# Performance work log

Hardware: AMD Instinct MI355X
Metric: run time of the kernel (lower is better)

The kernel has to match this reference:

```python
import jax, jax.numpy as jnp
import numpy as np

# Model hyperparameters (match init_kwargs)
C_IN = 256      # in_channels
H = 8           # n_heads
CH = 16         # hid_channels
FQ = 8          # freq_bins
WIN = 100       # window_size
VH = C_IN // H                  # 32, v_hid_channels
CT = H * (2 * CH + VH)          # 512, qkv conv out channels
HD = CH * FQ                    # 128, head_dim
VHD = VH * FQ                   # 256, v_head_dim
EPS = 1e-5


def _prelu(x, a):
    return jnp.where(x >= 0, x, a * x)


def _chan_ln(x, g, b):
    # LayerNormalization4D: normalize over channel dim (axis=1) of [B, Ch, D1, D2]
    mu = jnp.mean(x, axis=1, keepdims=True)
    var = jnp.var(x, axis=1, keepdims=True)
    return (x - mu) * jax.lax.rsqrt(var + EPS) * g[None, :, None, None] + b[None, :, None, None]


def setup_inputs() -> dict:
    key = jax.random.key(0)
    ks = jax.random.split(key, 8)
    B, T = 4, 1000
    x = jax.random.normal(ks[0], (B, C_IN, FQ, T), dtype=jnp.float32)
    w_qkv = jax.random.normal(ks[1], (CT, C_IN), dtype=jnp.float32) * 0.02
    b_qkv = jnp.zeros((CT,), dtype=jnp.float32)
    a_qkv = jnp.float32(0.25)
    g_qkv = jnp.ones((CT,), dtype=jnp.float32)
    be_qkv = jnp.zeros((CT,), dtype=jnp.float32)
    w_proj = jax.random.normal(ks[2], (C_IN, C_IN), dtype=jnp.float32) * 0.02
    b_proj = jnp.zeros((C_IN,), dtype=jnp.float32)
    a_proj = jnp.float32(0.25)
    g_proj = jnp.ones((C_IN,), dtype=jnp.float32)
    be_proj = jnp.zeros((C_IN,), dtype=jnp.float32)
    return {"x": x, "w_qkv": w_qkv, "b_qkv": b_qkv, "a_qkv": a_qkv, "g_qkv": g_qkv,
            "be_qkv": be_qkv, "w_proj": w_proj, "b_proj": b_proj, "a_proj": a_proj,
            "g_proj": g_proj, "be_proj": be_proj}


def reference(x, w_qkv, b_qkv, a_qkv, g_qkv, be_qkv, w_proj, b_proj, a_proj, g_proj, be_proj):
    B, C, F, T = x.shape
    # [B, C, F, T] -> [B, C, T, F]
    xt = jnp.swapaxes(x, -2, -1)
    # 1x1 conv2d (kernel_size=1) == channel matmul, then PReLU + channel LayerNorm
    h = jnp.einsum('oc,bctf->botf', w_qkv, xt) + b_qkv[None, :, None, None]
    h = _chan_ln(_prelu(h, a_qkv), g_qkv, be_qkv)          # [B, CT, T, F]
    # split into heads: [B, CT, T, F] -> [B, T, CT, F] -> [B, T, H, (2CH+VH)*F] -> [B, H, T, D]
    h = jnp.transpose(h, (0, 2, 1, 3)).reshape(B, T, H, -1)
    h = jnp.transpose(h, (0, 2, 1, 3))
    q = h[..., :HD]            # [B, H, T, HD]
    k = h[..., HD:2 * HD]      # [B, H, T, HD]
    v = h[..., 2 * HD:]        # [B, H, T, VHD]
    # sliding-window causal attention (training / non-cached branch, need_streaming=True)
    scores = jnp.einsum('bhtd,bhsd->bhts', q, k) * (HD ** -0.5)
    idx = jnp.arange(T)
    allowed = (idx[None, :] <= idx[:, None]) & (idx[None, :] >= idx[:, None] - WIN)
    scores = jnp.where(allowed[None, None], scores, jnp.float32(-jnp.inf))
    attn = jax.nn.softmax(scores, axis=-1)
    ctx = jnp.einsum('bhts,bhsv->bhtv', attn, v)           # [B, H, T, VHD]
    # [B, H, T, VHD] -> [B, H, VHD, T] -> [B, C, F, T]  (VHD = VH*F, H*VH = C)
    out = jnp.transpose(ctx, (0, 1, 3, 2)).reshape(B, C, F, T)
    # projection 1x1 conv + PReLU + channel LayerNorm
    out = jnp.einsum('oc,bcft->boft', w_proj, out) + b_proj[None, :, None, None]
    out = _chan_ln(_prelu(out, a_proj), g_proj, be_proj)
    return out
```

## Files before the change

### kernel.cpp

```cpp
#include <hip/hip_runtime.h>
#include <math.h>

#define T_DIM 1000

typedef __attribute__((ext_vector_type(8))) short short8;
typedef __attribute__((ext_vector_type(16))) float f32x16;

static __device__ __forceinline__ short bf16_rn(float f) {
  union { float f; unsigned u; } v;
  v.f = f;
  unsigned r = v.u + 0x7fffu + ((v.u >> 16) & 1u);
  return (short)(r >> 16);
}

__global__ __launch_bounds__(256) void cvt_bf16(const float* __restrict__ in,
                                                short* __restrict__ out,
                                                int n) {
  int i = blockIdx.x * 256 + threadIdx.x;
  if (i < n) out[i] = bf16_rn(in[i]);
}

__global__ __launch_bounds__(256) void xpose_x(const float* __restrict__ x,
                                               short* __restrict__ xbt) {
  __shared__ float tile[64][65];
  int bf = blockIdx.z;
  int b = bf >> 3, f = bf & 7;
  int c0 = blockIdx.x * 64, t0 = blockIdx.y * 64;
  int tid = threadIdx.x;
  int tc = tid & 63;
  int t = t0 + tc;
  if (t < T_DIM) {
    int sg = tid >> 6;
#pragma unroll
    for (int i = 0; i < 16; ++i) {
      int cr = i * 4 + sg;
      tile[cr][tc] = x[((size_t)(b * 256 + c0 + cr) * 8 + f) * T_DIM + t];
    }
  }
  __syncthreads();
  int tr = tid >> 2, cg = (tid & 3) * 16;
  int tt = t0 + tr;
  if (tt < T_DIM) {
    short tmp[16];
#pragma unroll
    for (int i = 0; i < 16; ++i) tmp[i] = bf16_rn(tile[cg + i][tr]);
    short* dst = xbt + ((size_t)((b * T_DIM + tt) * 8 + f)) * 256 + c0 + cg;
    *(short8*)dst = *(short8*)tmp;
    *(short8*)(dst + 8) = *(short8*)(tmp + 8);
  }
}

__global__ __launch_bounds__(512) void qkv_mfma(
    const short* __restrict__ xbt, const short* __restrict__ wb,
    const float* __restrict__ bias, const float* __restrict__ a_p,
    const float* __restrict__ gam, const float* __restrict__ bet,
    short* __restrict__ qkb, short* __restrict__ vpb) {
  __shared__ short Bs[64][264];
  __shared__ float lnS[8][2][32], lnQ[8][2][32];
  __shared__ float mu_s[2][32], ri_s[2][32];
  __shared__ float pb[512], pg[512], pe[512];
  int tid = threadIdx.x;
  int n0 = blockIdx.x * 64;
  int b = n0 / 8000;
  pb[tid] = bias[tid];
  pg[tid] = gam[tid];
  pe[tid] = bet[tid];
  {
    int row = tid >> 3, ch = tid & 7;
    const short8* src =
        (const short8*)(xbt + (size_t)(n0 + row) * 256 + ch * 32);
    *(short8*)&Bs[row][ch * 32] = src[0];
    *(short8*)&Bs[row][ch * 32 + 8] = src[1];
    *(short8*)&Bs[row][ch * 32 + 16] = src[2];
    *(short8*)&Bs[row][ch * 32 + 24] = src[3];
  }
  __syncthreads();
  int lane = tid & 63, wv = tid >> 6;
  int h = lane >> 5, l31 = lane & 31;
  int m0 = wv * 64;
  f32x16 acc[2][2];
#pragma unroll
  for (int mt = 0; mt < 2; ++mt)
#pragma unroll
    for (int nt = 0; nt < 2; ++nt)
#pragma unroll
      for (int r = 0; r < 16; ++r) acc[mt][nt][r] = 0.f;
  const short* wbase = wb + ((size_t)(m0 + l31)) * 256 + h * 8;
#pragma unroll
  for (int kk = 0; kk < 16; ++kk) {
    short8 bfr0 = *(const short8*)&Bs[l31][kk * 16 + h * 8];
    short8 bfr1 = *(const short8*)&Bs[32 + l31][kk * 16 + h * 8];
#pragma unroll
    for (int mt = 0; mt < 2; ++mt) {
      short8 af = *(const short8*)(wbase + (size_t)mt * 32 * 256 + kk * 16);
      acc[mt][0] =
          __builtin_amdgcn_mfma_f32_32x32x16_bf16(af, bfr0, acc[mt][0], 0, 0, 0);
      acc[mt][1] =
          __builtin_amdgcn_mfma_f32_32x32x16_bf16(af, bfr1, acc[mt][1], 0, 0, 0);
    }
  }
  float aslope = a_p[0];
  float sm[2] = {0.f, 0.f}, sq[2] = {0.f, 0.f};
#pragma unroll
  for (int mt = 0; mt < 2; ++mt) {
#pragma unroll
    for (int nt = 0; nt < 2; ++nt) {
#pragma unroll
      for (int r = 0; r < 16; ++r) {
        int row = (r & 3) + 8 * (r >> 2) + 4 * h;
        int o = m0 + mt * 32 + row;
        float v = acc[mt][nt][r] + pb[o];
        v = v >= 0.f ? v : aslope * v;
        acc[mt][nt][r] = v;
        sm[nt] += v;
        sq[nt] += v * v;
      }
    }
  }
#pragma unroll
  for (int nt = 0; nt < 2; ++nt) {
    sm[nt] += __shfl_xor(sm[nt], 32, 64);
    sq[nt] += __shfl_xor(sq[nt], 32, 64);
    if (h == 0) {
      lnS[wv][nt][l31] = sm[nt];
      lnQ[wv][nt][l31] = sq[nt];
    }
  }
  __syncthreads();
  if (tid < 64) {
    int nt = tid >> 5, c = tid & 31;
    float ss = 0.f, qq = 0.f;
#pragma unroll
    for (int w = 0; w < 8; ++w) {
      ss += lnS[w][nt][c];
      qq += lnQ[w][nt][c];
    }
    float mu = ss * (1.f / 512.f);
    float var = qq * (1.f / 512.f) - mu * mu;
    mu_s[nt][c] = mu;
    ri_s[nt][c] = rsqrtf(var + 1e-5f);
  }
  __syncthreads();
#pragma unroll
  for (int nt = 0; nt < 2; ++nt) {
    float mu = mu_s[nt][l31], ri = ri_s[nt][l31];
    int n = n0 + nt * 32 + l31;
    int t = (n >> 3) - b * T_DIM;
    int f = n & 7;
#pragma unroll
    for (int mt = 0; mt < 2; ++mt) {
#pragma unroll
      for (int r = 0; r < 16; ++r) {
        int row = (r & 3) + 8 * (r >> 2) + 4 * h;
        int o = m0 + mt * 32 + row;
        float v = (acc[mt][nt][r] - mu) * ri * pg[o] + pe[o];
        short bv = bf16_rn(v);
        int head = o >> 6, lo = o & 63;
        int bh = b * 8 + head;
        if (lo < 32) {
          qkb[((size_t)(bh * 32 + lo) * 1024 + t) * 8 + f] = bv;
        } else {
          vpb[((size_t)(bh * 128 + (t >> 3)) * 256 + f * 32 + (lo - 32)) * 8 +
              (t & 7)] = bv;
        }
      }
    }
  }
}

__global__ __launch_bounds__(256) void attn_mfma(const short* __restrict__ qkb,
                                                 const short* __restrict__ vpb,
                                                 short* __restrict__ ctxb) {
  __shared__ short pbuf[10][64 * 8];
  __shared__ float wmax[4][32], wsum[4][32];
  int bh = blockIdx.y;
  int qt0 = blockIdx.x * 32;
  int tid = threadIdx.x;
  int wv = tid >> 6, lane = tid & 63;
  int l31 = lane & 31, h = lane >> 5;
  int b = bh >> 3, hh = bh & 7;
  const short* qbase = qkb + (size_t)bh * 32 * 1024 * 8;
  short8 qf[8];
#pragma unroll
  for (int kk = 0; kk < 8; ++kk) {
    int qc = 2 * kk + h;
    qf[kk] = *(const short8*)(qbase + ((size_t)qc * 1024 + qt0 + l31) * 8);
  }
  int ks_lo = qt0 > 100 ? ((qt0 - 100) & ~31) : 0;
  int kt_n = (qt0 + 32 - ks_lo) >> 5;
  int kt0 = wv, kt1 = wv + 4;
  bool has0 = kt0 < kt_n, has1 = kt1 < kt_n;
  int q_t = qt0 + l31;
  f32x16 S0, S1;
  float pm = -INFINITY;
  if (has0) {
#pragma unroll
    for (int r = 0; r < 16; ++r) S0[r] = 0.f;
    int sb = ks_lo + kt0 * 32;
#pragma unroll
    for (int kk = 0; kk < 8; ++kk) {
      int kc = 16 + 2 * kk + h;
      short8 kf = *(const short8*)(qbase + ((size_t)kc * 1024 + sb + l31) * 8);
      S0 = __builtin_amdgcn_mfma_f32_32x32x16_bf16(kf, qf[kk], S0, 0, 0, 0);
    }
#pragma unroll
    for (int r = 0; r < 16; ++r) {
      int s = sb + (r & 3) + 8 * (r >> 2) + 4 * h;
      float v = S0[r] * 0.08838834764831843f;
      bool ok = (s <= q_t) && (s + 100 >= q_t);
      v = ok ? v : -INFINITY;
      S0[r] = v;
      pm = fmaxf(pm, v);
    }
  }
  if (has1) {
#pragma unroll
    for (int r = 0; r < 16; ++r) S1[r] = 0.f;
    int sb = ks_lo + kt1 * 32;
#pragma unroll
    for (int kk = 0; kk < 8; ++kk) {
      int kc = 16 + 2 * kk + h;
      short8 kf = *(const short8*)(qbase + ((size_t)kc * 1024 + sb + l31) * 8);
      S1 = __builtin_amdgcn_mfma_f32_32x32x16_bf16(kf, qf[kk], S1, 0, 0, 0);
    }
#pragma unroll
    for (int r = 0; r < 16; ++r) {
      int s = sb + (r & 3) + 8 * (r >> 2) + 4 * h;
      float v = S1[r] * 0.08838834764831843f;
      bool ok = (s <= q_t) && (s + 100 >= q_t);
      v = ok ? v : -INFINITY;
      S1[r] = v;
      pm = fmaxf(pm, v);
    }
  }
  pm = fmaxf(pm, __shfl_xor(pm, 32, 64));
  if (h == 0) wmax[wv][l31] = pm;
  __syncthreads();
  float gm = fmaxf(fmaxf(wmax[0][l31], wmax[1][l31]),
                   fmaxf(wmax[2][l31], wmax[3][l31]));
  float ws = 0.f;
  if (has0) {
#pragma unroll
    for (int r = 0; r < 16; ++r) {
      float e = __expf(S0[r] - gm);
      S0[r] = e;
      ws += e;
    }
  }
  if (has1) {
#pragma unroll
    for (int r = 0; r < 16; ++r) {
      float e = __expf(S1[r] - gm);
      S1[r] = e;
      ws += e;
    }
  }
  ws += __shfl_xor(ws, 32, 64);
  if (h == 0) wsum[wv][l31] = ws;
  __syncthreads();
  float inv =
      1.f / (wsum[0][l31] + wsum[1][l31] + wsum[2][l31] + wsum[3][l31]);
  if (has0) {
#pragma unroll
    for (int ks2 = 0; ks2 < 2; ++ks2) {
      short tmp8[8];
#pragma unroll
      for (int jj = 0; jj < 4; ++jj) {
        int rA = 8 * ks2 + jj, rB = rA + 4;
        short a16 = bf16_rn(S0[rA] * inv);
        short b16 = bf16_rn(S0[rB] * inv);
        int pk = (int)(unsigned short)a16 | (((int)b16) << 16);
        int xp = __shfl_xor(pk, 32, 64);
        tmp8[jj] = h == 0 ? a16 : (short)(xp >> 16);
        tmp8[4 + jj] = h == 0 ? (short)(xp & 0xffff) : b16;
      }
      *(short8*)&pbuf[kt0 * 2 + ks2][lane * 8] = *(short8*)tmp8;
    }
  }
  if (has1) {
#pragma unroll
    for (int ks2 = 0; ks2 < 2; ++ks2) {
      short tmp8[8];
#pragma unroll
      for (int jj = 0; jj < 4; ++jj) {
        int rA = 8 * ks2 + jj, rB = rA + 4;
        short a16 = bf16_rn(S1[rA] * inv);
        short b16 = bf16_rn(S1[rB] * inv);
        int pk = (int)(unsigned short)a16 | (((int)b16) << 16);
        int xp = __shfl_xor(pk, 32, 64);
        tmp8[jj] = h == 0 ? a16 : (short)(xp >> 16);
        tmp8[4 + jj] = h == 0 ? (short)(xp & 0xffff) : b16;
      }
      *(short8*)&pbuf[kt1 * 2 + ks2][lane * 8] = *(short8*)tmp8;
    }
  }
  __syncthreads();
  const short* vbase = vpb + (size_t)bh * 128 * 256 * 8;
#pragma unroll
  for (int j = 0; j < 2; ++j) {
    int nt = wv * 2 + j;
    f32x16 acc;
#pragma unroll
    for (int r = 0; r < 16; ++r) acc[r] = 0.f;
    for (int kt = 0; kt < kt_n; ++kt) {
#pragma unroll
      for (int ks2 = 0; ks2 < 2; ++ks2) {
        short8 pfr = *(const short8*)&pbuf[kt * 2 + ks2][lane * 8];
        int sb = ks_lo + kt * 32 + ks2 * 16 + h * 8;
        short8 vf = *(const short8*)(vbase +
                                     ((size_t)(sb >> 3) * 256 + nt * 32 + l31) * 8);
        acc = __builtin_amdgcn_mfma_f32_32x32x16_bf16(pfr, vf, acc, 0, 0, 0);
      }
    }
    short* crow = ctxb + ((size_t)(b * 8 + nt) * T_DIM) * 256 + hh * 32 + l31;
#pragma unroll
    for (int r = 0; r < 16; ++r) {
      int t = qt0 + (r & 3) + 8 * (r >> 2) + 4 * h;
      if (t < T_DIM) crow[(size_t)t * 256] = bf16_rn(acc[r]);
    }
  }
}

__global__ __launch_bounds__(256) void proj_mfma(
    const short* __restrict__ ctxb, const short* __restrict__ wb,
    const float* __restrict__ bias, const float* __restrict__ a_p,
    const float* __restrict__ gam, const float* __restrict__ bet,
    float* __restrict__ out) {
  __shared__ short Bs[64][264];
  __shared__ float lnS[4][2][32], lnQ[4][2][32];
  __shared__ float mu_s[2][32], ri_s[2][32];
  __shared__ float pb[256], pg[256], pe[256];
  int tid = threadIdx.x;
  int blk = blockIdx.x;
  int bf = blk >> 4, tb = blk & 15;
  int b = bf >> 3, f = bf & 7;
  int t0 = tb * 64;
  pb[tid] = bias[tid];
  pg[tid] = gam[tid];
  pe[tid] = bet[tid];
  {
    int row = tid >> 2, seg = (tid & 3) * 64;
    int t = t0 + row;
    if (t < T_DIM) {
      const short8* src =
          (const short8*)(ctxb + ((size_t)bf * T_DIM + t) * 256 + seg);
#pragma unroll
      for (int j = 0; j < 8; ++j) *(short8*)&Bs[row][seg + 8 * j] = src[j];
    } else {
      short8 z = {0, 0, 0, 0, 0, 0, 0, 0};
#pragma unroll
      for (int j = 0; j < 8; ++j) *(short8*)&Bs[row][seg + 8 * j] = z;
    }
  }
  __syncthreads();
  int lane = tid & 63, wv = tid >> 6;
  int h = lane >> 5, l31 = lane & 31;
  int m0 = wv * 64;
  f32x16 acc[2][2];
#pragma unroll
  for (int mt = 0; mt < 2; ++mt)
#pragma unroll
    for (int nt = 0; nt < 2; ++nt)
#pragma unroll
      for (int r = 0; r < 16; ++r) acc[mt][nt][r] = 0.f;
  const short* wbase = wb + ((size_t)(m0 + l31)) * 256 + h * 8;
#pragma unroll
  for (int kk = 0; kk < 16; ++kk) {
    short8 bfr0 = *(const short8*)&Bs[l31][kk * 16 + h * 8];
    short8 bfr1 = *(const short8*)&Bs[32 + l31][kk * 16 + h * 8];
#pragma unroll
    for (int mt = 0; mt < 2; ++mt) {
      short8 af = *(const short8*)(wbase + (size_t)mt * 32 * 256 + kk * 16);
      acc[mt][0] =
          __builtin_amdgcn_mfma_f32_32x32x16_bf16(af, bfr0, acc[mt][0], 0, 0, 0);
      acc[mt][1] =
          __builtin_amdgcn_mfma_f32_32x32x16_bf16(af, bfr1, acc[mt][1], 0, 0, 0);
    }
  }
  float aslope = a_p[0];
  float sm[2] = {0.f, 0.f}, sq[2] = {0.f, 0.f};
#pragma unroll
  for (int mt = 0; mt < 2; ++mt) {
#pragma unroll
    for (int nt = 0; nt < 2; ++nt) {
#pragma unroll
      for (int r = 0; r < 16; ++r) {
        int row = (r & 3) + 8 * (r >> 2) + 4 * h;
        int o = m0 + mt * 32 + row;
        float v = acc[mt][nt][r] + pb[o];
        v = v >= 0.f ? v : aslope * v;
        acc[mt][nt][r] = v;
        sm[nt] += v;
        sq[nt] += v * v;
      }
    }
  }
#pragma unroll
  for (int nt = 0; nt < 2; ++nt) {
    sm[nt] += __shfl_xor(sm[nt], 32, 64);
    sq[nt] += __shfl_xor(sq[nt], 32, 64);
    if (h == 0) {
      lnS[wv][nt][l31] = sm[nt];
      lnQ[wv][nt][l31] = sq[nt];
    }
  }
  __syncthreads();
  if (tid < 64) {
    int nt = tid >> 5, c = tid & 31;
    float ss = lnS[0][nt][c] + lnS[1][nt][c] + lnS[2][nt][c] + lnS[3][nt][c];
    float qq = lnQ[0][nt][c] + lnQ[1][nt][c] + lnQ[2][nt][c] + lnQ[3][nt][c];
    float mu = ss * (1.f / 256.f);
    float var = qq * (1.f / 256.f) - mu * mu;
    mu_s[nt][c] = mu;
    ri_s[nt][c] = rsqrtf(var + 1e-5f);
  }
  __syncthreads();
#pragma unroll
  for (int nt = 0; nt < 2; ++nt) {
    float mu = mu_s[nt][l31], ri = ri_s[nt][l31];
    int t = t0 + nt * 32 + l31;
    if (t < T_DIM) {
#pragma unroll
      for (int mt = 0; mt < 2; ++mt) {
#pragma unroll
        for (int r = 0; r < 16; ++r) {
          int row = (r & 3) + 8 * (r >> 2) + 4 * h;
          int o = m0 + mt * 32 + row;
          float v = (acc[mt][nt][r] - mu) * ri * pg[o] + pe[o];
          out[((size_t)(b * 2048 + o * 8 + f)) * T_DIM + t] = v;
        }
      }
    }
  }
}

extern "C" void kernel_launch(void* const* d_in, const int* in_sizes, int n_in,
                              void* d_out, int out_size, void* d_ws,
                              size_t ws_size, hipStream_t stream) {
  const float* x = (const float*)d_in[0];
  const float* w_qkv = (const float*)d_in[1];
  const float* b_qkv = (const float*)d_in[2];
  const float* a_qkv = (const float*)d_in[3];
  const float* g_qkv = (const float*)d_in[4];
  const float* be_qkv = (const float*)d_in[5];
  const float* w_proj = (const float*)d_in[6];
  const float* b_proj = (const float*)d_in[7];
  const float* a_proj = (const float*)d_in[8];
  const float* g_proj = (const float*)d_in[9];
  const float* be_proj = (const float*)d_in[10];
  float* out = (float*)d_out;

  short* wqb = (short*)d_ws;
  short* wpb = wqb + 131072;
  short* xbt = wpb + 65536;
  short* qkb = xbt + (size_t)8192000;
  short* vpb = qkb + (size_t)8388608;
  short* ctxb = vpb + (size_t)8388608;

  cvt_bf16<<<512, 256, 0, stream>>>(w_qkv, wqb, 512 * 256);
  cvt_bf16<<<256, 256, 0, stream>>>(w_proj, wpb, 256 * 256);
  xpose_x<<<dim3(4, 16, 32), 256, 0, stream>>>(x, xbt);
  qkv_mfma<<<500, 512, 0, stream>>>(xbt, wqb, b_qkv, a_qkv, g_qkv, be_qkv,
                                    qkb, vpb);
  attn_mfma<<<dim3(32, 32), 256, 0, stream>>>(qkb, vpb, ctxb);
  proj_mfma<<<512, 256, 0, stream>>>(ctxb, wpb, b_proj, a_proj, g_proj,
                                     be_proj, out);
}
```

Before: 184.3 us.

## Fuse input transpose and bf16 cast into QKV GEMM, merge weight casts

Removes the separate transpose kernel and the intermediate bf16 transposed copy of x. The QKV kernel now reads fp32 x directly, converts it to bf16, and packs it into shared memory. The two weight conversion launches are merged into one, and the grid index mapping of the attention and projection kernels is swapped so that neighbouring blocks cover different batch/heads. This saves a global round trip and two launches, at the cost of strided fp32 loads and 32-bit LDS stores inside the GEMM prologue.

```diff
diff --git a/kernel.cpp b/kernel.cpp
--- a/kernel.cpp
+++ b/kernel.cpp
@@ -13,45 +13,18 @@
   return (short)(r >> 16);
 }
 
-__global__ __launch_bounds__(256) void cvt_bf16(const float* __restrict__ in,
-                                                short* __restrict__ out,
-                                                int n) {
+__global__ __launch_bounds__(256) void prep_w(const float* __restrict__ wq,
+                                              const float* __restrict__ wp,
+                                              short* __restrict__ wqb,
+                                              short* __restrict__ wpb) {
   int i = blockIdx.x * 256 + threadIdx.x;
-  if (i < n) out[i] = bf16_rn(in[i]);
-}
-
-__global__ __launch_bounds__(256) void xpose_x(const float* __restrict__ x,
-                                               short* __restrict__ xbt) {
-  __shared__ float tile[64][65];
-  int bf = blockIdx.z;
-  int b = bf >> 3, f = bf & 7;
-  int c0 = blockIdx.x * 64, t0 = blockIdx.y * 64;
-  int tid = threadIdx.x;
-  int tc = tid & 63;
-  int t = t0 + tc;
-  if (t < T_DIM) {
-    int sg = tid >> 6;
-#pragma unroll
-    for (int i = 0; i < 16; ++i) {
-      int cr = i * 4 + sg;
-      tile[cr][tc] = x[((size_t)(b * 256 + c0 + cr) * 8 + f) * T_DIM + t];
-    }
-  }
-  __syncthreads();
-  int tr = tid >> 2, cg = (tid & 3) * 16;
-  int tt = t0 + tr;
-  if (tt < T_DIM) {
-    short tmp[16];
-#pragma unroll
-    for (int i = 0; i < 16; ++i) tmp[i] = bf16_rn(tile[cg + i][tr]);
-    short* dst = xbt + ((size_t)((b * T_DIM + tt) * 8 + f)) * 256 + c0 + cg;
-    *(short8*)dst = *(short8*)tmp;
-    *(short8*)(dst + 8) = *(short8*)(tmp + 8);
-  }
+  if (i < 131072) wqb[i] = bf16_rn(wq[i]);
+  int j = i - 131072;
+  if (j >= 0 && j < 65536) wpb[j] = bf16_rn(wp[j]);
 }
 
 __global__ __launch_bounds__(512) void qkv_mfma(
-    const short* __restrict__ xbt, const short* __restrict__ wb,
+    const float* __restrict__ x, const short* __restrict__ wb,
     const float* __restrict__ bias, const float* __restrict__ a_p,
     const float* __restrict__ gam, const float* __restrict__ bet,
     short* __restrict__ qkb, short* __restrict__ vpb) {
@@ -60,19 +33,34 @@
   __shared__ float mu_s[2][32], ri_s[2][32];
   __shared__ float pb[512], pg[512], pe[512];
   int tid = threadIdx.x;
-  int n0 = blockIdx.x * 64;
-  int b = n0 / 8000;
+  int blk = blockIdx.x;
+  int b = blk / 125;
+  int t0 = (blk * 8) % 1000;
   pb[tid] = bias[tid];
   pg[tid] = gam[tid];
   pe[tid] = bet[tid];
   {
-    int row = tid >> 3, ch = tid & 7;
-    const short8* src =
-        (const short8*)(xbt + (size_t)(n0 + row) * 256 + ch * 32);
-    *(short8*)&Bs[row][ch * 32] = src[0];
-    *(short8*)&Bs[row][ch * 32 + 8] = src[1];
-    *(short8*)&Bs[row][ch * 32 + 16] = src[2];
-    *(short8*)&Bs[row][ch * 32 + 24] = src[3];
+    const float* xb = x + (size_t)b * 256 * 8000 + t0;
+#pragma unroll
+    for (int i = 0; i < 2; ++i) {
+      int u = tid + i * 512;
+      int f = u & 7, cp = u >> 3;
+      int c0 = cp * 2;
+      const float* pa = xb + ((size_t)c0 * 8 + f) * 1000;
+      const float* pbx = xb + ((size_t)(c0 + 1) * 8 + f) * 1000;
+      float4 va0 = *(const float4*)pa;
+      float4 va1 = *(const float4*)(pa + 4);
+      float4 vb0 = *(const float4*)pbx;
+      float4 vb1 = *(const float4*)(pbx + 4);
+      float fa[8] = {va0.x, va0.y, va0.z, va0.w, va1.x, va1.y, va1.z, va1.w};
+      float fb[8] = {vb0.x, vb0.y, vb0.z, vb0.w, vb1.x, vb1.y, vb1.z, vb1.w};
+#pragma unroll
+      for (int tt = 0; tt < 8; ++tt) {
+        unsigned lo = (unsigned short)bf16_rn(fa[tt]);
+        unsigned hi = (unsigned short)bf16_rn(fb[tt]);
+        *(unsigned*)&Bs[tt * 8 + f][c0] = lo | (hi << 16);
+      }
+    }
   }
   __syncthreads();
   int lane = tid & 63, wv = tid >> 6;
@@ -144,9 +132,8 @@
 #pragma unroll
   for (int nt = 0; nt < 2; ++nt) {
     float mu = mu_s[nt][l31], ri = ri_s[nt][l31];
-    int n = n0 + nt * 32 + l31;
-    int t = (n >> 3) - b * T_DIM;
-    int f = n & 7;
+    int tg = t0 + ((nt * 32 + l31) >> 3);
+    int f = (nt * 32 + l31) & 7;
 #pragma unroll
     for (int mt = 0; mt < 2; ++mt) {
 #pragma unroll
@@ -158,10 +145,10 @@
         int head = o >> 6, lo = o & 63;
         int bh = b * 8 + head;
         if (lo < 32) {
-          qkb[((size_t)(bh * 32 + lo) * 1024 + t) * 8 + f] = bv;
+          qkb[((size_t)(bh * 32 + lo) * 1024 + tg) * 8 + f] = bv;
         } else {
-          vpb[((size_t)(bh * 128 + (t >> 3)) * 256 + f * 32 + (lo - 32)) * 8 +
-              (t & 7)] = bv;
+          vpb[((size_t)(bh * 128 + (tg >> 3)) * 256 + f * 32 + (lo - 32)) * 8 +
+              (tg & 7)] = bv;
         }
       }
     }
@@ -173,8 +160,8 @@
                                                  short* __restrict__ ctxb) {
   __shared__ short pbuf[10][64 * 8];
   __shared__ float wmax[4][32], wsum[4][32];
-  int bh = blockIdx.y;
-  int qt0 = blockIdx.x * 32;
+  int bh = blockIdx.x;
+  int qt0 = blockIdx.y * 32;
   int tid = threadIdx.x;
   int wv = tid >> 6, lane = tid & 63;
   int l31 = lane & 31, h = lane >> 5;
@@ -332,7 +319,7 @@
   __shared__ float pb[256], pg[256], pe[256];
   int tid = threadIdx.x;
   int blk = blockIdx.x;
-  int bf = blk >> 4, tb = blk & 15;
+  int bf = blk & 31, tb = blk >> 5;
   int b = bf >> 3, f = bf & 7;
   int t0 = tb * 64;
   pb[tid] = bias[tid];
@@ -452,15 +439,12 @@
 
   short* wqb = (short*)d_ws;
   short* wpb = wqb + 131072;
-  short* xbt = wpb + 65536;
-  short* qkb = xbt + (size_t)8192000;
+  short* qkb = wpb + 65536;
   short* vpb = qkb + (size_t)8388608;
   short* ctxb = vpb + (size_t)8388608;
 
-  cvt_bf16<<<512, 256, 0, stream>>>(w_qkv, wqb, 512 * 256);
-  cvt_bf16<<<256, 256, 0, stream>>>(w_proj, wpb, 256 * 256);
-  xpose_x<<<dim3(4, 16, 32), 256, 0, stream>>>(x, xbt);
-  qkv_mfma<<<500, 512, 0, stream>>>(xbt, wqb, b_qkv, a_qkv, g_qkv, be_qkv,
+  prep_w<<<768, 256, 0, stream>>>(w_qkv, w_proj, wqb, wpb);
+  qkv_mfma<<<500, 512, 0, stream>>>(x, wqb, b_qkv, a_qkv, g_qkv, be_qkv,
                                     qkb, vpb);
   attn_mfma<<<dim3(32, 32), 256, 0, stream>>>(qkb, vpb, ctxb);
   proj_mfma<<<512, 256, 0, stream>>>(ctxb, wpb, b_proj, a_proj, g_proj,
```

Measured after the change: 175.6 us. 1.05x faster.
